# Performance work log

Measured on AMD Instinct MI355X. Metric: run time of the kernel, lower is better.

## Reference

```python
import jax, jax.numpy as jnp
import numpy as np

B, S, D, H = 2, 2048, 1024, 16
DK = D // H
ROPE_BASE = 10000.0


def _rope_tables(seq_len, dim):
    # [S, dim] cos/sin tables, matching torch cat([freqs, freqs], -1)
    inv_freq = 1.0 / (ROPE_BASE ** (jnp.arange(0, dim, 2, dtype=jnp.float32) / dim))
    freqs = jnp.arange(seq_len, dtype=jnp.float32)[:, None] * inv_freq[None, :]
    emb = jnp.concatenate([freqs, freqs], axis=-1)
    return jnp.cos(emb), jnp.sin(emb)


def _rotate_half(x):
    x1, x2 = x[..., : x.shape[-1] // 2], x[..., x.shape[-1] // 2 :]
    return jnp.concatenate([-x2, x1], axis=-1)


def setup_inputs() -> dict:
    key = jax.random.key(0)
    ks = jax.random.split(key, 8)
    q = jax.random.normal(ks[0], (B, S, D), jnp.float32)
    k = jax.random.normal(ks[1], (B, S, D), jnp.float32)
    v = jax.random.normal(ks[2], (B, S, D), jnp.float32)
    mask = jnp.tril(jnp.ones((S, S), jnp.int32))[None, None]  # causal [1,1,S,S]
    scale = 0.02
    Wq = jax.random.normal(ks[3], (D, D), jnp.float32) * scale
    Wk = jax.random.normal(ks[4], (D, D), jnp.float32) * scale
    Wv = jax.random.normal(ks[5], (D, D), jnp.float32) * scale
    Wo = jax.random.normal(ks[6], (D, D), jnp.float32) * scale
    bq = jnp.zeros((D,), jnp.float32)
    bk = jnp.zeros((D,), jnp.float32)
    bv = jnp.zeros((D,), jnp.float32)
    bo = jnp.zeros((D,), jnp.float32)
    return {"q": q, "k": k, "v": v, "mask": mask,
            "Wq": Wq, "bq": bq, "Wk": Wk, "bk": bk,
            "Wv": Wv, "bv": bv, "Wo": Wo, "bo": bo}


def reference(q, k, v, mask, Wq, bq, Wk, bk, Wv, bv, Wo, bo):
    b, s, d = q.shape
    # QKV projections, reshape to [B, H, S, d_k]
    query = (q @ Wq + bq).reshape(b, s, H, DK).transpose(0, 2, 1, 3)
    key_ = (k @ Wk + bk).reshape(b, s, H, DK).transpose(0, 2, 1, 3)
    value = (v @ Wv + bv).reshape(b, s, H, DK).transpose(0, 2, 1, 3)
    # RoPE on q and k
    cos, sin = _rope_tables(s, DK)  # [S, DK]
    cos = cos[None, None]
    sin = sin[None, None]
    query = query * cos + _rotate_half(query) * sin
    key_ = key_ * cos + _rotate_half(key_) * sin
    # scaled dot-product attention with mask-fill
    scores = jnp.einsum("bhqd,bhkd->bhqk", query, key_) / jnp.sqrt(jnp.float32(DK))
    scores = jnp.where(mask == 0, jnp.float32(-1e9), scores)
    attn = jax.nn.softmax(scores, axis=-1)
    out = jnp.einsum("bhqk,bhkd->bhqd", attn, value)  # [B,H,S,DK]
    out = out.transpose(0, 2, 1, 3).reshape(b, s, d)
    return out @ Wo + bo
```

## Files before the change

### kernel.cpp

```cpp
#include <hip/hip_runtime.h>
#include <hip/hip_bf16.h>
#include <math.h>

#define Bb 2
#define Ss 2048
#define Dd 1024
#define Hh 16
#define DKk 64
#define BSn (Bb*Ss)

typedef unsigned short u16;
typedef __attribute__((ext_vector_type(8))) short frag_ab;
typedef __attribute__((ext_vector_type(4))) float frag_cd;

static __device__ __forceinline__ u16 f2bf(float x) {
    __hip_bfloat16 h = __float2bfloat16(x);
    return *reinterpret_cast<u16*>(&h);
}

static __device__ __forceinline__ void gload16(const u16* g, u16* l) {
    __builtin_amdgcn_global_load_lds(
        (const __attribute__((address_space(1))) void*)g,
        (__attribute__((address_space(3))) void*)l, 16, 0, 0);
}

__global__ __launch_bounds__(256)
void convert_kernel(const float* __restrict__ q, const float* __restrict__ k,
                    const float* __restrict__ v,
                    const float* __restrict__ Wq, const float* __restrict__ Wk,
                    const float* __restrict__ Wv, const float* __restrict__ Wo,
                    u16* __restrict__ qb, u16* __restrict__ kb, u16* __restrict__ vb,
                    u16* __restrict__ wqt, u16* __restrict__ wkt,
                    u16* __restrict__ wvt, u16* __restrict__ wot)
{
    __shared__ u16 T[64 * 80];
    const int tid = threadIdx.x;
    const int bid = blockIdx.x;
    if (bid < 3072) {
        int t = bid >> 10;
        const float* src = (t == 0) ? q : (t == 1) ? k : v;
        u16* dst = (t == 0) ? qb : (t == 1) ? kb : vb;
        size_t base = (size_t)(bid & 1023) * 4096;
#pragma unroll
        for (int i = 0; i < 4; ++i) {
            size_t e = base + (size_t)(tid + i * 256) * 4;
            float4 xv = *(const float4*)(src + e);
            ushort4 o;
            o.x = f2bf(xv.x); o.y = f2bf(xv.y); o.z = f2bf(xv.z); o.w = f2bf(xv.w);
            *(ushort4*)(dst + e) = o;
        }
    } else {
        int wbid = bid - 3072;
        int w = wbid >> 8;
        const float* src = (w == 0) ? Wq : (w == 1) ? Wk : (w == 2) ? Wv : Wo;
        u16* dst = (w == 0) ? wqt : (w == 1) ? wkt : (w == 2) ? wvt : wot;
        int t = wbid & 255;
        int k0 = (t >> 4) * 64, nt0 = (t & 15) * 64;
#pragma unroll
        for (int i = 0; i < 4; ++i) {
            int f = tid + i * 256;
            int kk = f >> 4, nn = (f & 15) * 4;
            float4 xv = *(const float4*)(src + (size_t)(k0 + kk) * Dd + nt0 + nn);
            T[(nn + 0) * 80 + kk] = f2bf(xv.x);
            T[(nn + 1) * 80 + kk] = f2bf(xv.y);
            T[(nn + 2) * 80 + kk] = f2bf(xv.z);
            T[(nn + 3) * 80 + kk] = f2bf(xv.w);
        }
        __syncthreads();
#pragma unroll
        for (int i = 0; i < 2; ++i) {
            int g = tid + i * 256;
            int nn = g >> 3, k8 = (g & 7) * 8;
            *(uint4*)(dst + (size_t)(nt0 + nn) * Dd + k0 + k8) =
                *(const uint4*)&T[nn * 80 + k8];
        }
    }
}

__global__ __launch_bounds__(256)
void gemm_bf16(const u16* __restrict__ X0, const u16* __restrict__ X1,
               const u16* __restrict__ X2,
               const u16* __restrict__ W0, const u16* __restrict__ W1,
               const u16* __restrict__ W2,
               const float* __restrict__ b0, const float* __restrict__ b1,
               const float* __restrict__ b2,
               u16* __restrict__ O0, u16* __restrict__ O1, u16* __restrict__ O2,
               float* __restrict__ OutF, int fused)
{
    __shared__ u16 As[128 * 64];
    __shared__ u16 Bs[64 * 64];

    const int tid = threadIdx.x;
    const int wv = tid >> 6, lane = tid & 63, l16 = lane & 15, quad = lane >> 4;
    const int n0 = blockIdx.x * 64, m0 = blockIdx.y * 128;
    const int z = blockIdx.z;

    const u16* X      = fused ? ((z == 0) ? X0 : (z == 1) ? X1 : X2) : X0;
    const u16* Wt     = fused ? ((z == 0) ? W0 : (z == 1) ? W1 : W2) : W0;
    const float* bias = fused ? ((z == 0) ? b0 : (z == 1) ? b1 : b2) : b0;
    u16* OutB         = (z == 0) ? O0 : (z == 1) ? O1 : O2;
    const int mode    = fused ? ((z == 0) ? 1 : (z == 1) ? 3 : 2) : 0;

    const int srow = tid >> 3;
    const int scol = (tid & 7) * 8;

    frag_cd acc[2][4];
#pragma unroll
    for (int ms = 0; ms < 2; ++ms)
#pragma unroll
        for (int n = 0; n < 4; ++n) acc[ms][n] = (frag_cd){0.f, 0.f, 0.f, 0.f};

    for (int k0 = 0; k0 < Dd; k0 += 64) {
        __syncthreads();
#pragma unroll
        for (int p = 0; p < 4; ++p)
            gload16(&X[(size_t)(m0 + p * 32 + srow) * Dd + k0 + scol],
                    &As[p * 2048 + wv * 512]);
#pragma unroll
        for (int p = 0; p < 2; ++p)
            gload16(&Wt[(size_t)(n0 + p * 32 + srow) * Dd + k0 + scol],
                    &Bs[p * 2048 + wv * 512]);
        __syncthreads();

#pragma unroll
        for (int ks = 0; ks < 2; ++ks) {
            frag_ab a0 = *(const frag_ab*)&As[(wv * 32 + l16) * 64 + ks * 32 + quad * 8];
            frag_ab a1 = *(const frag_ab*)&As[(wv * 32 + 16 + l16) * 64 + ks * 32 + quad * 8];
#pragma unroll
            for (int n = 0; n < 4; ++n) {
                frag_ab b = *(const frag_ab*)&Bs[(n * 16 + l16) * 64 + ks * 32 + quad * 8];
                acc[0][n] = __builtin_amdgcn_mfma_f32_16x16x32_bf16(a0, b, acc[0][n], 0, 0, 0);
                acc[1][n] = __builtin_amdgcn_mfma_f32_16x16x32_bf16(a1, b, acc[1][n], 0, 0, 0);
            }
        }
    }

    float bv4[4];
#pragma unroll
    for (int n = 0; n < 4; ++n) bv4[n] = bias[n0 + n * 16 + l16];

    if (mode == 0) {
#pragma unroll
        for (int ms = 0; ms < 2; ++ms)
#pragma unroll
            for (int r = 0; r < 4; ++r) {
                int row = m0 + wv * 32 + ms * 16 + quad * 4 + r;
#pragma unroll
                for (int n = 0; n < 4; ++n)
                    OutF[(size_t)row * Dd + n0 + n * 16 + l16] = acc[ms][n][r] + bv4[n];
            }
    } else if (mode == 2) {
        const int h = n0 >> 6;
        const int b = m0 >> 11;
#pragma unroll
        for (int ms = 0; ms < 2; ++ms) {
            int sbase = (m0 & (Ss - 1)) + wv * 32 + ms * 16 + quad * 4;
#pragma unroll
            for (int n = 0; n < 4; ++n) {
                int d = n * 16 + l16;
                ushort4 o;
                o.x = f2bf(acc[ms][n][0] + bv4[n]);
                o.y = f2bf(acc[ms][n][1] + bv4[n]);
                o.z = f2bf(acc[ms][n][2] + bv4[n]);
                o.w = f2bf(acc[ms][n][3] + bv4[n]);
                *(ushort4*)&OutB[(((size_t)b * Hh + h) * DKk + d) * Ss + sbase] = o;
            }
        }
    } else {
        const int h = n0 >> 6;
        const float lg = 0.28782313662425575f;
        const float sc = (mode == 1) ? 0.125f : 1.0f;
#pragma unroll
        for (int ms = 0; ms < 2; ++ms)
#pragma unroll
            for (int r = 0; r < 4; ++r) {
                int row = m0 + wv * 32 + ms * 16 + quad * 4 + r;
                int b = row >> 11, s = row & (Ss - 1);
                u16* orow = OutB + (((size_t)b * Hh + h) * Ss + s) * DKk;
#pragma unroll
                for (int n = 0; n < 2; ++n) {
                    int j = n * 16 + l16;
                    float ang = (float)s * __expf(-(float)j * lg);
                    float cv = cosf(ang), sv = sinf(ang);
                    float lo = acc[ms][n][r] + bv4[n];
                    float hi = acc[ms][n + 2][r] + bv4[n + 2];
                    orow[j]      = f2bf((lo * cv - hi * sv) * sc);
                    orow[j + 32] = f2bf((hi * cv + lo * sv) * sc);
                }
            }
    }
}

__global__ __launch_bounds__(256)
void gemm_out(const u16* __restrict__ X0, const u16* __restrict__ W0,
              const float* __restrict__ b0, float* __restrict__ OutF)
{
    __shared__ u16 As[64 * 64];
    __shared__ u16 Bs[64 * 64];

    const int tid = threadIdx.x;
    const int wv = tid >> 6, lane = tid & 63, l16 = lane & 15, quad = lane >> 4;
    const int n0 = blockIdx.x * 64, m0 = blockIdx.y * 64;

    const int srow = tid >> 3;
    const int scol = (tid & 7) * 8;

    frag_cd acc[4];
#pragma unroll
    for (int n = 0; n < 4; ++n) acc[n] = (frag_cd){0.f, 0.f, 0.f, 0.f};

    for (int k0 = 0; k0 < Dd; k0 += 64) {
        __syncthreads();
#pragma unroll
        for (int p = 0; p < 2; ++p) {
            gload16(&X0[(size_t)(m0 + p * 32 + srow) * Dd + k0 + scol],
                    &As[p * 2048 + wv * 512]);
            gload16(&W0[(size_t)(n0 + p * 32 + srow) * Dd + k0 + scol],
                    &Bs[p * 2048 + wv * 512]);
        }
        __syncthreads();

#pragma unroll
        for (int ks = 0; ks < 2; ++ks) {
            frag_ab a0 = *(const frag_ab*)&As[(wv * 16 + l16) * 64 + ks * 32 + quad * 8];
#pragma unroll
            for (int n = 0; n < 4; ++n) {
                frag_ab b = *(const frag_ab*)&Bs[(n * 16 + l16) * 64 + ks * 32 + quad * 8];
                acc[n] = __builtin_amdgcn_mfma_f32_16x16x32_bf16(a0, b, acc[n], 0, 0, 0);
            }
        }
    }

    float bv4[4];
#pragma unroll
    for (int n = 0; n < 4; ++n) bv4[n] = b0[n0 + n * 16 + l16];

#pragma unroll
    for (int r = 0; r < 4; ++r) {
        int row = m0 + wv * 16 + quad * 4 + r;
#pragma unroll
        for (int n = 0; n < 4; ++n)
            OutF[(size_t)row * Dd + n0 + n * 16 + l16] = acc[n][r] + bv4[n];
    }
}

__global__ __launch_bounds__(256)
void attn_mfma(const u16* __restrict__ Q, const u16* __restrict__ K,
               const u16* __restrict__ Vt, u16* __restrict__ Aout)
{
    __shared__ u16 Qs[64 * 72];
    __shared__ u16 Ks[64 * 64];
    __shared__ u16 Vs[64 * 64];
    __shared__ u16 Ps[64 * 72];

    const int tid = threadIdx.x;
    const int wv = tid >> 6;
    const int lane = tid & 63;
    const int l16 = lane & 15;
    const int quad = lane >> 4;

    const int bh = blockIdx.y;
    const int vsw = (blockIdx.x + (bh & 7)) & 31;
    const int jj  = bh >> 3;
    const int qb  = (jj == 0) ? vsw
                  : (jj == 1) ? ((vsw + 8) & 31)
                  : (jj == 2) ? ((23 - vsw) & 31)
                  :             (31 - vsw);
    const int q0 = qb * 64;

    const size_t qkbase = (size_t)bh * Ss * DKk;
    const size_t vbase  = (size_t)bh * DKk * Ss;
    const int b = bh >> 4, h = bh & 15;

    const int srow = tid >> 3;
    const int scol = ((tid & 7) ^ (srow & 7)) * 8;
    const int sx   = (l16 & 7) * 8;

#pragma unroll
    for (int rep = 0; rep < 2; ++rep) {
        int g = tid + rep * 256;
        int row = g >> 3, c8 = (g & 7) * 8;
        *(uint4*)&Qs[row * 72 + c8] =
            *(const uint4*)&Q[qkbase + (size_t)(q0 + row) * DKk + c8];
    }

    float m_r[4], l_r[4];
#pragma unroll
    for (int r = 0; r < 4; ++r) { m_r[r] = -3.0e38f; l_r[r] = 0.f; }
    frag_cd of[4];
#pragma unroll
    for (int n = 0; n < 4; ++n) of[n] = (frag_cd){0.f, 0.f, 0.f, 0.f};

    for (int kb = 0; kb <= qb; ++kb) {
        const int k0 = kb * 64;
        __syncthreads();
#pragma unroll
        for (int p = 0; p < 2; ++p) {
            gload16(&K[qkbase + (size_t)(k0 + p * 32 + srow) * DKk + scol],
                    &Ks[p * 2048 + wv * 512]);
            gload16(&Vt[vbase + (size_t)(p * 32 + srow) * Ss + k0 + scol],
                    &Vs[p * 2048 + wv * 512]);
        }
        __syncthreads();

        frag_cd sf[4];
#pragma unroll
        for (int n = 0; n < 4; ++n) sf[n] = (frag_cd){0.f, 0.f, 0.f, 0.f};
#pragma unroll
        for (int h2 = 0; h2 < 2; ++h2) {
            frag_ab qa = *(const frag_ab*)&Qs[(wv * 16 + l16) * 72 + h2 * 32 + quad * 8];
#pragma unroll
            for (int n = 0; n < 4; ++n) {
                frag_ab kf = *(const frag_ab*)&Ks[(n * 16 + l16) * 64 + ((h2 * 32 + quad * 8) ^ sx)];
                sf[n] = __builtin_amdgcn_mfma_f32_16x16x32_bf16(qa, kf, sf[n], 0, 0, 0);
            }
        }

        if (kb == qb) {
#pragma unroll
            for (int r = 0; r < 4; ++r) {
                int qi = wv * 16 + quad * 4 + r;
#pragma unroll
                for (int n = 0; n < 4; ++n)
                    if (n * 16 + l16 > qi) sf[n][r] = -1.0e30f;
            }
        }

        float alpha[4];
#pragma unroll
        for (int r = 0; r < 4; ++r) {
            float mx = m_r[r];
#pragma unroll
            for (int n = 0; n < 4; ++n) mx = fmaxf(mx, sf[n][r]);
#pragma unroll
            for (int off = 1; off < 16; off <<= 1) mx = fmaxf(mx, __shfl_xor(mx, off));
            float a = __expf(m_r[r] - mx);
            m_r[r] = mx;
            float sum = 0.f;
#pragma unroll
            for (int n = 0; n < 4; ++n) {
                float p = __expf(sf[n][r] - mx);
                sf[n][r] = p;
                sum += p;
            }
#pragma unroll
            for (int off = 1; off < 16; off <<= 1) sum += __shfl_xor(sum, off);
            l_r[r] = l_r[r] * a + sum;
            alpha[r] = a;
        }
#pragma unroll
        for (int n = 0; n < 4; ++n)
#pragma unroll
            for (int r = 0; r < 4; ++r) of[n][r] *= alpha[r];

#pragma unroll
        for (int n = 0; n < 4; ++n)
#pragma unroll
            for (int r = 0; r < 4; ++r)
                Ps[(wv * 16 + quad * 4 + r) * 72 + n * 16 + l16] = f2bf(sf[n][r]);
        __threadfence_block();

#pragma unroll
        for (int h2 = 0; h2 < 2; ++h2) {
            frag_ab pa = *(const frag_ab*)&Ps[(wv * 16 + l16) * 72 + h2 * 32 + quad * 8];
#pragma unroll
            for (int n = 0; n < 4; ++n) {
                frag_ab vf = *(const frag_ab*)&Vs[(n * 16 + l16) * 64 + ((h2 * 32 + quad * 8) ^ sx)];
                of[n] = __builtin_amdgcn_mfma_f32_16x16x32_bf16(pa, vf, of[n], 0, 0, 0);
            }
        }
    }

#pragma unroll
    for (int r = 0; r < 4; ++r) {
        float inv = 1.f / l_r[r];
        int row = q0 + wv * 16 + quad * 4 + r;
        u16* orow = Aout + ((size_t)b * Ss + row) * Dd + h * DKk;
#pragma unroll
        for (int n = 0; n < 4; ++n) orow[n * 16 + l16] = f2bf(of[n][r] * inv);
    }
}

extern "C" void kernel_launch(void* const* d_in, const int* in_sizes, int n_in,
                              void* d_out, int out_size, void* d_ws, size_t ws_size,
                              hipStream_t stream) {
    (void)in_sizes; (void)n_in; (void)out_size;
    const float* q  = (const float*)d_in[0];
    const float* k  = (const float*)d_in[1];
    const float* v  = (const float*)d_in[2];
    const float* Wq = (const float*)d_in[4];
    const float* bq = (const float*)d_in[5];
    const float* Wk = (const float*)d_in[6];
    const float* bk = (const float*)d_in[7];
    const float* Wv = (const float*)d_in[8];
    const float* bv = (const float*)d_in[9];
    const float* Wo = (const float*)d_in[10];
    const float* bo = (const float*)d_in[11];
    float* out = (float*)d_out;

    const size_t E = (size_t)Bb * Ss * Dd;
    const size_t Wn = (size_t)Dd * Dd;
    const size_t need = (7 * E + 4 * Wn) * sizeof(u16);
    if (ws_size < need) return;
    u16* qa  = (u16*)d_ws;
    u16* ka  = qa + E;
    u16* va  = ka + E;
    u16* wqt = va + E;
    u16* wkt = wqt + Wn;
    u16* wvt = wkt + Wn;
    u16* wot = wvt + Wn;
    u16* Qh  = wot + Wn;
    u16* Kh  = Qh + E;
    u16* Vth = Kh + E;
    u16* Abf = Vth + E;

    convert_kernel<<<4096, 256, 0, stream>>>(q, k, v, Wq, Wk, Wv, Wo,
                                             qa, ka, va, wqt, wkt, wvt, wot);
    gemm_bf16<<<dim3(Dd / 64, BSn / 128, 3), 256, 0, stream>>>(
        qa, ka, va, wqt, wkt, wvt, bq, bk, bv, Qh, Kh, Vth, nullptr, 1);
    attn_mfma<<<dim3(32, Bb * Hh), 256, 0, stream>>>(Qh, Kh, Vth, Abf);
    gemm_out<<<dim3(Dd / 64, BSn / 64), 256, 0, stream>>>(Abf, wot, bo, out);
}
```

Baseline: 274.8 us.

## Double-buffer K/V tiles in attention and keep Q fragments in registers

The attention kernel now double-buffers the K and V tiles in shared memory. The next block's async global-to-LDS loads are issued right after the barrier, so they overlap with the current block's MFMA and softmax work, and one barrier per iteration is dropped. Q fragments are loaded straight into registers instead of being staged through shared memory. The P tile switches from padded rows to an XOR swizzle to avoid bank conflicts. LDS use rises for the extra buffers, and correctness depends on the barrier draining the outstanding async loads.

```diff
diff --git a/kernel.cpp b/kernel.cpp
--- a/kernel.cpp
+++ b/kernel.cpp
@@ -248,10 +248,9 @@
 void attn_mfma(const u16* __restrict__ Q, const u16* __restrict__ K,
                const u16* __restrict__ Vt, u16* __restrict__ Aout)
 {
-    __shared__ u16 Qs[64 * 72];
-    __shared__ u16 Ks[64 * 64];
-    __shared__ u16 Vs[64 * 64];
-    __shared__ u16 Ps[64 * 72];
+    __shared__ u16 Ks[2][64 * 64];
+    __shared__ u16 Vs[2][64 * 64];
+    __shared__ u16 Ps[64 * 64];
 
     const int tid = threadIdx.x;
     const int wv = tid >> 6;
@@ -276,12 +275,20 @@
     const int scol = ((tid & 7) ^ (srow & 7)) * 8;
     const int sx   = (l16 & 7) * 8;
 
-#pragma unroll
-    for (int rep = 0; rep < 2; ++rep) {
-        int g = tid + rep * 256;
-        int row = g >> 3, c8 = (g & 7) * 8;
-        *(uint4*)&Qs[row * 72 + c8] =
-            *(const uint4*)&Q[qkbase + (size_t)(q0 + row) * DKk + c8];
+    frag_ab qreg[2];
+    {
+        const u16* qrow = &Q[qkbase + (size_t)(q0 + wv * 16 + l16) * DKk];
+#pragma unroll
+        for (int h2 = 0; h2 < 2; ++h2)
+            qreg[h2] = *(const frag_ab*)&qrow[h2 * 32 + quad * 8];
+    }
+
+#pragma unroll
+    for (int p = 0; p < 2; ++p) {
+        gload16(&K[qkbase + (size_t)(p * 32 + srow) * DKk + scol],
+                &Ks[0][p * 2048 + wv * 512]);
+        gload16(&Vt[vbase + (size_t)(p * 32 + srow) * Ss + scol],
+                &Vs[0][p * 2048 + wv * 512]);
     }
 
     float m_r[4], l_r[4];
@@ -292,27 +299,32 @@
     for (int n = 0; n < 4; ++n) of[n] = (frag_cd){0.f, 0.f, 0.f, 0.f};
 
     for (int kb = 0; kb <= qb; ++kb) {
-        const int k0 = kb * 64;
-        __syncthreads();
-#pragma unroll
-        for (int p = 0; p < 2; ++p) {
-            gload16(&K[qkbase + (size_t)(k0 + p * 32 + srow) * DKk + scol],
-                    &Ks[p * 2048 + wv * 512]);
-            gload16(&Vt[vbase + (size_t)(p * 32 + srow) * Ss + k0 + scol],
-                    &Vs[p * 2048 + wv * 512]);
-        }
-        __syncthreads();
+        const int cur = kb & 1;
+        const u16* KsB = Ks[cur];
+        const u16* VsB = Vs[cur];
+
+        __syncthreads();
+
+        if (kb < qb) {
+            const int k0n = (kb + 1) * 64;
+#pragma unroll
+            for (int p = 0; p < 2; ++p) {
+                gload16(&K[qkbase + (size_t)(k0n + p * 32 + srow) * DKk + scol],
+                        &Ks[cur ^ 1][p * 2048 + wv * 512]);
+                gload16(&Vt[vbase + (size_t)(p * 32 + srow) * Ss + k0n + scol],
+                        &Vs[cur ^ 1][p * 2048 + wv * 512]);
+            }
+        }
 
         frag_cd sf[4];
 #pragma unroll
         for (int n = 0; n < 4; ++n) sf[n] = (frag_cd){0.f, 0.f, 0.f, 0.f};
 #pragma unroll
         for (int h2 = 0; h2 < 2; ++h2) {
-            frag_ab qa = *(const frag_ab*)&Qs[(wv * 16 + l16) * 72 + h2 * 32 + quad * 8];
-#pragma unroll
-            for (int n = 0; n < 4; ++n) {
-                frag_ab kf = *(const frag_ab*)&Ks[(n * 16 + l16) * 64 + ((h2 * 32 + quad * 8) ^ sx)];
-                sf[n] = __builtin_amdgcn_mfma_f32_16x16x32_bf16(qa, kf, sf[n], 0, 0, 0);
+#pragma unroll
+            for (int n = 0; n < 4; ++n) {
+                frag_ab kf = *(const frag_ab*)&KsB[(n * 16 + l16) * 64 + ((h2 * 32 + quad * 8) ^ sx)];
+                sf[n] = __builtin_amdgcn_mfma_f32_16x16x32_bf16(qreg[h2], kf, sf[n], 0, 0, 0);
             }
         }
 
@@ -356,16 +368,18 @@
 #pragma unroll
         for (int n = 0; n < 4; ++n)
 #pragma unroll
-            for (int r = 0; r < 4; ++r)
-                Ps[(wv * 16 + quad * 4 + r) * 72 + n * 16 + l16] = f2bf(sf[n][r]);
+            for (int r = 0; r < 4; ++r) {
+                int row = wv * 16 + quad * 4 + r;
+                Ps[row * 64 + ((n * 16 + l16) ^ ((row & 7) << 3))] = f2bf(sf[n][r]);
+            }
         __threadfence_block();
 
 #pragma unroll
         for (int h2 = 0; h2 < 2; ++h2) {
-            frag_ab pa = *(const frag_ab*)&Ps[(wv * 16 + l16) * 72 + h2 * 32 + quad * 8];
-#pragma unroll
-            for (int n = 0; n < 4; ++n) {
-                frag_ab vf = *(const frag_ab*)&Vs[(n * 16 + l16) * 64 + ((h2 * 32 + quad * 8) ^ sx)];
+            frag_ab pa = *(const frag_ab*)&Ps[(wv * 16 + l16) * 64 + ((h2 * 32 + quad * 8) ^ sx)];
+#pragma unroll
+            for (int n = 0; n < 4; ++n) {
+                frag_ab vf = *(const frag_ab*)&VsB[(n * 16 + l16) * 64 + ((h2 * 32 + quad * 8) ^ sx)];
                 of[n] = __builtin_amdgcn_mfma_f32_16x16x32_bf16(pa, vf, of[n], 0, 0, 0);
             }
         }
```

New measurement: 274.4 us. No clear change (-0.2%).
